# Kernel tuning notes

Measured on AMD Instinct MI355X. Metric: run time of the kernel, lower is better.

Reference implementation:

```python
import jax, jax.numpy as jnp
import numpy as np

HEADS = 16
DIM_HEAD = 64
DIM = 1024
DIM_HIDDEN = HEADS * DIM_HEAD


def setup_inputs() -> dict:
    key = jax.random.key(0)
    ks = jax.random.split(key, 5)
    b, n = 4, 2048
    x = jax.random.normal(ks[0], (b, n, DIM), dtype=jnp.float32)
    # nn.Linear weights stored as [out, in]; init ~ U(-1/sqrt(in), 1/sqrt(in))
    s = 1.0 / np.sqrt(DIM)
    w_q = jax.random.uniform(ks[1], (DIM_HIDDEN, DIM), minval=-s, maxval=s, dtype=jnp.float32)
    w_kv = jax.random.uniform(ks[2], (2 * DIM_HIDDEN, DIM), minval=-s, maxval=s, dtype=jnp.float32)
    so = 1.0 / np.sqrt(DIM_HIDDEN)
    w_out = jax.random.uniform(ks[3], (DIM, DIM_HIDDEN), minval=-so, maxval=so, dtype=jnp.float32)
    b_out = jax.random.uniform(ks[4], (DIM,), minval=-so, maxval=so, dtype=jnp.float32)
    return {"x": x, "w_q": w_q, "w_kv": w_kv, "w_out": w_out, "b_out": b_out}


def reference(x, w_q, w_kv, w_out, b_out):
    b, n, _ = x.shape
    h, e = HEADS, DIM_HEAD
    q = x @ w_q.T                     # [b, n, h*e]
    kv = x @ w_kv.T                   # [b, n, 2*h*e]
    k, v = jnp.split(kv, 2, axis=-1)
    split = lambda t: t.reshape(b, n, h, e).transpose(0, 2, 1, 3)  # [b, h, n, e]
    q, k, v = split(q), split(k), split(v)
    scale = e ** (-0.5)
    energy = jnp.einsum('bhie,bhje->bhij', q, k) * scale
    attn_w = jax.nn.softmax(energy, axis=-1)
    attn = jnp.einsum('bhij,bhje->bhie', attn_w, v)  # [b, h, n, e]
    out = attn.transpose(0, 2, 1, 3).reshape(b, n, h * e)
    return out @ w_out.T + b_out
```

## Files before the change

kernel.cpp:

```cpp
#include <hip/hip_runtime.h>

typedef __attribute__((ext_vector_type(8))) short bf16x8;
typedef __attribute__((ext_vector_type(4))) float f32x4;

#define AS1 __attribute__((address_space(1)))
#define AS3 __attribute__((address_space(3)))

#if defined(__has_builtin)
#  if __has_builtin(__builtin_amdgcn_exp2f)
#    define EXP2F(x) __builtin_amdgcn_exp2f(x)
#  endif
#endif
#ifndef EXP2F
#  define EXP2F(x) __builtin_exp2f(x)
#endif

#define BAR_WAIT_VM8  asm volatile("s_waitcnt vmcnt(8)\ns_barrier" ::: "memory")
#define BAR_WAIT_VM4  asm volatile("s_waitcnt vmcnt(4)\ns_barrier" ::: "memory")
#define BAR_WAIT_VM2  asm volatile("s_waitcnt vmcnt(2)\ns_barrier" ::: "memory")
#define BAR_WAIT_VM0  asm volatile("s_waitcnt vmcnt(0)\ns_barrier" ::: "memory")
#define BAR_WAIT_LGKM asm volatile("s_waitcnt lgkmcnt(0)\ns_barrier" ::: "memory")

#define PL32(a, b) asm("v_permlane32_swap_b32 %0, %1" : "+v"(a), "+v"(b))
#define PL16(a, b) asm("v_permlane16_swap_b32 %0, %1" : "+v"(a), "+v"(b))

__device__ __forceinline__ unsigned short f2bf(float f) {
    union { float f; unsigned u; } v; v.f = f;
    unsigned r = v.u + 0x7fffu + ((v.u >> 16) & 1u);
    return (unsigned short)(r >> 16);
}

__device__ __forceinline__ void dma16(const void* g, void* l) {
    __builtin_amdgcn_global_load_lds((const AS1 unsigned int*)g,
                                     (AS3 unsigned int*)l, 16, 0, 0);
}

__global__ __launch_bounds__(256) void convert_regions(
    const float* __restrict__ s0, unsigned short* __restrict__ d0, int n0, float c0,
    const float* __restrict__ s1, unsigned short* __restrict__ d1, int n1, float c1,
    const float* __restrict__ s2, unsigned short* __restrict__ d2, int n2, float c2)
{
    long long e = ((long long)blockIdx.x * 256 + threadIdx.x) * 8;
    const float* s; unsigned short* d; float sc;
    if (e < n0) { s = s0; d = d0; sc = c0; }
    else { e -= n0;
    if (e < n1) { s = s1; d = d1; sc = c1; }
    else { e -= n1;
    if (e < n2) { s = s2; d = d2; sc = c2; } else return; } }
    const float4 f0 = *(const float4*)(s + e);
    const float4 f1 = *(const float4*)(s + e + 4);
    union { unsigned short u[8]; uint4 q; } t;
    t.u[0]=f2bf(f0.x*sc); t.u[1]=f2bf(f0.y*sc); t.u[2]=f2bf(f0.z*sc); t.u[3]=f2bf(f0.w*sc);
    t.u[4]=f2bf(f1.x*sc); t.u[5]=f2bf(f1.y*sc); t.u[6]=f2bf(f1.z*sc); t.u[7]=f2bf(f1.w*sc);
    *(uint4*)(d + e) = t.q;
}

template<int CM>
__global__ __launch_bounds__(256) void gemm128(
    const unsigned short* __restrict__ A, const unsigned short* __restrict__ B,
    void* __restrict__ C0, void* __restrict__ C1, void* __restrict__ C2,
    const float* __restrict__ bias, int M, int N, int K)
{
    __shared__ __align__(16) unsigned short smem[2 * 16384];

    const int tid  = threadIdx.x;
    const int wq   = tid >> 6;
    const int lane = tid & 63;
    const int l16  = lane & 15;
    const int quad = lane >> 4;
    const int m0   = blockIdx.x * 128;
    const int n0   = blockIdx.y * 128;
    const int lr   = lane >> 3;
    const int cs   = lane & 7;
    const bool vswap = (CM == 1) && (n0 >= 2048);

    f32x4 acc[4][4];
#pragma unroll
    for (int mt = 0; mt < 4; ++mt)
#pragma unroll
        for (int nt = 0; nt < 4; ++nt) acc[mt][nt] = (f32x4){0.f, 0.f, 0.f, 0.f};

    auto issue = [&](int buf, int kk) {
        unsigned short* as = smem + buf * 16384;
        unsigned short* bs = as + 8192;
#pragma unroll
        for (int i = 0; i < 4; ++i) {
            const int rr = (wq * 4 + i) * 8 + lr;
            const int cg = cs ^ (rr & 7);
            dma16(A + (size_t)(m0 + rr) * K + kk + cg * 8, as + (wq * 4 + i) * 512);
            dma16(B + (size_t)(n0 + rr) * K + kk + cg * 8, bs + (wq * 4 + i) * 512);
        }
    };

    const int nIt = K >> 6;
    issue(0, 0);
#pragma unroll 2
    for (int it = 0; it < nIt; ++it) {
        const int cur = it & 1;
        if (it + 1 < nIt) {
            issue(cur ^ 1, (it + 1) << 6);
            BAR_WAIT_VM8;
        } else {
            BAR_WAIT_VM0;
        }
        const unsigned short* as = smem + cur * 16384;
        const unsigned short* bs = as + 8192;
#pragma unroll
        for (int ch = 0; ch < 2; ++ch) {
            const int swz = (((ch * 4 + quad) ^ (l16 & 7)) * 8);
            bf16x8 aF[4], bF[4];
#pragma unroll
            for (int mt = 0; mt < 4; ++mt)
                aF[mt] = *(const bf16x8*)(as + ((wq >> 1) * 64 + mt * 16 + l16) * 64 + swz);
#pragma unroll
            for (int nt = 0; nt < 4; ++nt)
                bF[nt] = *(const bf16x8*)(bs + ((wq & 1) * 64 + nt * 16 + l16) * 64 + swz);
            if (vswap) {
#pragma unroll
                for (int mt = 0; mt < 4; ++mt)
#pragma unroll
                    for (int nt = 0; nt < 4; ++nt)
                        acc[mt][nt] = __builtin_amdgcn_mfma_f32_16x16x32_bf16(
                            bF[nt], aF[mt], acc[mt][nt], 0, 0, 0);
            } else {
#pragma unroll
                for (int mt = 0; mt < 4; ++mt)
#pragma unroll
                    for (int nt = 0; nt < 4; ++nt)
                        acc[mt][nt] = __builtin_amdgcn_mfma_f32_16x16x32_bf16(
                            aF[mt], bF[nt], acc[mt][nt], 0, 0, 0);
            }
        }
        BAR_WAIT_LGKM;
    }

    const int wr = wq >> 1, wc = wq & 1;
    if (CM == 0) {
#pragma unroll
        for (int mt = 0; mt < 4; ++mt)
#pragma unroll
        for (int nt = 0; nt < 4; ++nt) {
            const int coln = n0 + wc * 64 + nt * 16 + l16;
            const float bv = bias ? bias[coln] : 0.f;
#pragma unroll
            for (int r = 0; r < 4; ++r) {
                const int rowm = m0 + wr * 64 + mt * 16 + quad * 4 + r;
                ((float*)C0)[(size_t)rowm * N + coln] = acc[mt][nt][r] + bv;
            }
        }
    } else if (!vswap) {
#pragma unroll
        for (int mt = 0; mt < 4; ++mt)
#pragma unroll
        for (int nt = 0; nt < 4; ++nt) {
            const int coln = n0 + wc * 64 + nt * 16 + l16;
            unsigned short* dst = (coln < 1024) ? (unsigned short*)C0 : (unsigned short*)C1;
            const int h = (coln >> 6) & 15, e = coln & 63;
#pragma unroll
            for (int r = 0; r < 4; ++r) {
                const int rowm = m0 + wr * 64 + mt * 16 + quad * 4 + r;
                const int b = rowm >> 11, n = rowm & 2047;
                dst[(((size_t)(b * 16 + h) * 2048 + n) << 6) + e] = f2bf(acc[mt][nt][r]);
            }
        }
    } else {
#pragma unroll
        for (int mt = 0; mt < 4; ++mt)
#pragma unroll
        for (int nt = 0; nt < 4; ++nt) {
#pragma unroll
            for (int r = 0; r < 4; ++r) {
                const int eg = n0 + wc * 64 + nt * 16 + quad * 4 + r;
                const int h = (eg >> 6) - 32, e = eg & 63;
                const int rowm = m0 + wr * 64 + mt * 16 + l16;
                const int b = rowm >> 11, n = rowm & 2047;
                ((unsigned short*)C2)[((size_t)(b * 16 + h) * 64 + e) * 2048 + n] =
                    f2bf(acc[mt][nt][r]);
            }
        }
    }
}

__global__ __launch_bounds__(512, 4) void attn_kernel(
    const unsigned short* __restrict__ Q, const unsigned short* __restrict__ K,
    const unsigned short* __restrict__ V, unsigned short* __restrict__ O)
{
    __shared__ __align__(16) unsigned short KVs[2 * 8192];

    const int tid  = threadIdx.x;
    const int q0   = blockIdx.x * 256;
    const int bh   = blockIdx.y;
    const int wq   = tid >> 6;
    const int lane = tid & 63;
    const int l16  = lane & 15;
    const int quad = lane >> 4;
    const int lr   = lane >> 3;
    const int cs   = lane & 7;
    const int swl  = l16 & 7;

    const unsigned short* Qg = Q + (size_t)bh * 2048 * 64;
    const unsigned short* Kg = K + (size_t)bh * 2048 * 64;
    const unsigned short* Vg = V + (size_t)bh * 64 * 2048;

    bf16x8 bQ[2][2];
#pragma unroll
    for (int sub = 0; sub < 2; ++sub)
#pragma unroll
        for (int ch = 0; ch < 2; ++ch)
            bQ[sub][ch] = *(const bf16x8*)(Qg + (size_t)(q0 + wq * 32 + sub * 16 + l16) * 64
                                           + ch * 32 + quad * 8);

    bf16x8 ones;
#pragma unroll
    for (int i = 0; i < 8; ++i) ones[i] = (short)0x3F80;

    f32x4 o[2][4], lf[2];
#pragma unroll
    for (int s = 0; s < 2; ++s) {
        lf[s] = (f32x4){0.f, 0.f, 0.f, 0.f};
#pragma unroll
        for (int e = 0; e < 4; ++e) o[s][e] = (f32x4){0.f, 0.f, 0.f, 0.f};
    }

    auto issueKV = [&](int buf, int key0) {
        unsigned short* ks = KVs + buf * 8192;
        unsigned short* vt = ks + 4096;
#pragma unroll
        for (int i = 0; i < 2; ++i) {
            const int j  = wq * 2 + i;
            const int rr = (j & 7) * 8 + lr;
            const int cg = cs ^ (rr & 7);
            if (j < 8)
                dma16(Kg + (size_t)(key0 + rr) * 64 + cg * 8, ks + (j & 7) * 512);
            else
                dma16(Vg + (size_t)rr * 2048 + key0 + cg * 8, vt + (j & 7) * 512);
        }
    };

    issueKV(0, 0);
#pragma unroll 2
    for (int kt = 0; kt < 32; ++kt) {
        const int cur = kt & 1;
        if (kt + 1 < 32) {
            issueKV(cur ^ 1, (kt + 1) * 64);
            BAR_WAIT_VM2;
        } else {
            BAR_WAIT_VM0;
        }
        const unsigned short* ks = KVs + cur * 8192;
        const unsigned short* vt = ks + 4096;

        f32x4 s[2][4];
#pragma unroll
        for (int sub = 0; sub < 2; ++sub)
#pragma unroll
            for (int c = 0; c < 4; ++c) s[sub][c] = (f32x4){0.f, 0.f, 0.f, 0.f};
#pragma unroll
        for (int ch = 0; ch < 2; ++ch) {
            const int swz = ((ch * 4 + quad) ^ swl) * 8;
#pragma unroll
            for (int c = 0; c < 4; ++c) {
                const bf16x8 aK = *(const bf16x8*)(ks + (c * 16 + l16) * 64 + swz);
#pragma unroll
                for (int sub = 0; sub < 2; ++sub)
                    s[sub][c] = __builtin_amdgcn_mfma_f32_16x16x32_bf16(
                        aK, bQ[sub][ch], s[sub][c], 0, 0, 0);
            }
        }

        bf16x8 aP[2][2];
#pragma unroll
        for (int sub = 0; sub < 2; ++sub) {
            unsigned pkx[4], pky[4];
#pragma unroll
            for (int c = 0; c < 4; ++c) {
                const float p0 = EXP2F(s[sub][c][0]);
                const float p1 = EXP2F(s[sub][c][1]);
                const float p2 = EXP2F(s[sub][c][2]);
                const float p3 = EXP2F(s[sub][c][3]);
                pkx[c] = __builtin_amdgcn_perm(__float_as_uint(p1), __float_as_uint(p0), 0x07060302);
                pky[c] = __builtin_amdgcn_perm(__float_as_uint(p3), __float_as_uint(p2), 0x07060302);
            }
#pragma unroll
            for (int cc = 0; cc < 2; ++cc) {
                unsigned dx = pkx[cc * 2], ex = pkx[cc * 2 + 1];
                unsigned dy = pky[cc * 2], ey = pky[cc * 2 + 1];
                PL32(dx, ex); PL32(dy, ey);
                PL16(dx, ex); PL16(dy, ey);
                union { unsigned u[4]; bf16x8 v; } t;
                t.u[0] = dx; t.u[1] = dy; t.u[2] = ex; t.u[3] = ey;
                aP[sub][cc] = t.v;
            }
        }

#pragma unroll
        for (int cc = 0; cc < 2; ++cc) {
            const int swz = ((cc * 4 + quad) ^ swl) * 8;
#pragma unroll
            for (int sub = 0; sub < 2; ++sub)
                lf[sub] = __builtin_amdgcn_mfma_f32_16x16x32_bf16(aP[sub][cc], ones, lf[sub], 0, 0, 0);
#pragma unroll
            for (int et = 0; et < 4; ++et) {
                const bf16x8 bV = *(const bf16x8*)(vt + (et * 16 + l16) * 64 + swz);
#pragma unroll
                for (int sub = 0; sub < 2; ++sub)
                    o[sub][et] = __builtin_amdgcn_mfma_f32_16x16x32_bf16(
                        aP[sub][cc], bV, o[sub][et], 0, 0, 0);
            }
        }
        BAR_WAIT_LGKM;
    }

    const int bb = bh >> 4, hh = bh & 15;
#pragma unroll
    for (int sub = 0; sub < 2; ++sub) {
#pragma unroll
        for (int r = 0; r < 4; ++r) {
            const float linv = 1.0f / lf[sub][r];
            const int qrow = q0 + wq * 32 + sub * 16 + quad * 4 + r;
#pragma unroll
            for (int et = 0; et < 4; ++et) {
                O[(size_t)(bb * 2048 + qrow) * 1024 + hh * 64 + et * 16 + l16] =
                    f2bf(o[sub][et][r] * linv);
            }
        }
    }
}

extern "C" void kernel_launch(void* const* d_in, const int* in_sizes, int n_in,
                              void* d_out, int out_size, void* d_ws, size_t ws_size,
                              hipStream_t stream) {
    const float* x     = (const float*)d_in[0];
    const float* w_q   = (const float*)d_in[1];
    const float* w_kv  = (const float*)d_in[2];
    const float* w_out = (const float*)d_in[3];
    const float* b_out = (const float*)d_in[4];
    const float CEXP = 0.125f * 1.44269504f;
    const size_t MB = 1024 * 1024;

    unsigned short* Qw    = (unsigned short*)d_ws;
    unsigned short* Kw    = (unsigned short*)((char*)d_ws + 16 * MB);
    unsigned short* Vw    = (unsigned short*)((char*)d_ws + 32 * MB);
    unsigned short* Ow    = (unsigned short*)((char*)d_ws + 48 * MB);
    unsigned short* xb    = (unsigned short*)d_out;
    unsigned short* wqkvb = (unsigned short*)((char*)d_out + 16 * MB);
    unsigned short* wob   = Qw;

    convert_regions<<<5632, 256, 0, stream>>>(
        x, xb, 8388608, 1.0f,
        w_q, wqkvb, 1048576, CEXP,
        w_kv, wqkvb + (size_t)1048576, 2097152, 1.0f);

    gemm128<1><<<dim3(64, 24), 256, 0, stream>>>(
        xb, wqkvb, Qw, Kw, Vw, nullptr, 8192, 3072, 1024);

    attn_kernel<<<dim3(8, 64), 512, 0, stream>>>(Qw, Kw, Vw, Ow);

    convert_regions<<<512, 256, 0, stream>>>(
        w_out, wob, 1048576, 1.0f,
        nullptr, nullptr, 0, 0.f, nullptr, nullptr, 0, 0.f);

    gemm128<0><<<dim3(64, 8), 256, 0, stream>>>(
        Ow, wob, d_out, nullptr, nullptr, b_out, 8192, 1024, 1024);
}
```

Before: 242.8 us.

## Halve attention query tile per block and remap grid for XCD-aware head locality

The attention kernel now handles 128 query rows per block (16 per wave) instead of 256, which doubles the grid to 1024 blocks and halves per-wave accumulator registers. Occupancy hints rise from 4 to 6 blocks. A 1D grid is decoded so that consecutive block IDs map to different heads in a pattern meant to keep blocks of the same head on the same XCD for K/V cache reuse. The cost is twice the K/V loads per query and fewer MFMAs per LDS read of K and V.

```diff
diff --git a/kernel.cpp b/kernel.cpp
--- a/kernel.cpp
+++ b/kernel.cpp
@@ -181,15 +181,18 @@
     }
 }
 
-__global__ __launch_bounds__(512, 4) void attn_kernel(
+__global__ __launch_bounds__(512, 6) void attn_kernel(
     const unsigned short* __restrict__ Q, const unsigned short* __restrict__ K,
     const unsigned short* __restrict__ V, unsigned short* __restrict__ O)
 {
     __shared__ __align__(16) unsigned short KVs[2 * 8192];
 
     const int tid  = threadIdx.x;
-    const int q0   = blockIdx.x * 256;
-    const int bh   = blockIdx.y;
+    const int id   = blockIdx.x;
+    const int r_   = id & 7;
+    const int s_   = id >> 3;
+    const int q0   = (s_ & 15) * 128;
+    const int bh   = r_ + 8 * (s_ >> 4);
     const int wq   = tid >> 6;
     const int lane = tid & 63;
     const int l16  = lane & 15;
@@ -202,25 +205,19 @@
     const unsigned short* Kg = K + (size_t)bh * 2048 * 64;
     const unsigned short* Vg = V + (size_t)bh * 64 * 2048;
 
-    bf16x8 bQ[2][2];
-#pragma unroll
-    for (int sub = 0; sub < 2; ++sub)
-#pragma unroll
-        for (int ch = 0; ch < 2; ++ch)
-            bQ[sub][ch] = *(const bf16x8*)(Qg + (size_t)(q0 + wq * 32 + sub * 16 + l16) * 64
-                                           + ch * 32 + quad * 8);
+    bf16x8 bQ[2];
+#pragma unroll
+    for (int ch = 0; ch < 2; ++ch)
+        bQ[ch] = *(const bf16x8*)(Qg + (size_t)(q0 + wq * 16 + l16) * 64 + ch * 32 + quad * 8);
 
     bf16x8 ones;
 #pragma unroll
     for (int i = 0; i < 8; ++i) ones[i] = (short)0x3F80;
 
-    f32x4 o[2][4], lf[2];
-#pragma unroll
-    for (int s = 0; s < 2; ++s) {
-        lf[s] = (f32x4){0.f, 0.f, 0.f, 0.f};
-#pragma unroll
-        for (int e = 0; e < 4; ++e) o[s][e] = (f32x4){0.f, 0.f, 0.f, 0.f};
-    }
+    f32x4 o[4], lf;
+    lf = (f32x4){0.f, 0.f, 0.f, 0.f};
+#pragma unroll
+    for (int e = 0; e < 4; ++e) o[e] = (f32x4){0.f, 0.f, 0.f, 0.f};
 
     auto issueKV = [&](int buf, int key0) {
         unsigned short* ks = KVs + buf * 8192;
@@ -250,34 +247,28 @@
         const unsigned short* ks = KVs + cur * 8192;
         const unsigned short* vt = ks + 4096;
 
-        f32x4 s[2][4];
-#pragma unroll
-        for (int sub = 0; sub < 2; ++sub)
-#pragma unroll
-            for (int c = 0; c < 4; ++c) s[sub][c] = (f32x4){0.f, 0.f, 0.f, 0.f};
+        f32x4 s4[4];
+#pragma unroll
+        for (int c = 0; c < 4; ++c) s4[c] = (f32x4){0.f, 0.f, 0.f, 0.f};
 #pragma unroll
         for (int ch = 0; ch < 2; ++ch) {
             const int swz = ((ch * 4 + quad) ^ swl) * 8;
 #pragma unroll
             for (int c = 0; c < 4; ++c) {
                 const bf16x8 aK = *(const bf16x8*)(ks + (c * 16 + l16) * 64 + swz);
-#pragma unroll
-                for (int sub = 0; sub < 2; ++sub)
-                    s[sub][c] = __builtin_amdgcn_mfma_f32_16x16x32_bf16(
-                        aK, bQ[sub][ch], s[sub][c], 0, 0, 0);
-            }
-        }
-
-        bf16x8 aP[2][2];
-#pragma unroll
-        for (int sub = 0; sub < 2; ++sub) {
+                s4[c] = __builtin_amdgcn_mfma_f32_16x16x32_bf16(aK, bQ[ch], s4[c], 0, 0, 0);
+            }
+        }
+
+        bf16x8 aP[2];
+        {
             unsigned pkx[4], pky[4];
 #pragma unroll
             for (int c = 0; c < 4; ++c) {
-                const float p0 = EXP2F(s[sub][c][0]);
-                const float p1 = EXP2F(s[sub][c][1]);
-                const float p2 = EXP2F(s[sub][c][2]);
-                const float p3 = EXP2F(s[sub][c][3]);
+                const float p0 = EXP2F(s4[c][0]);
+                const float p1 = EXP2F(s4[c][1]);
+                const float p2 = EXP2F(s4[c][2]);
+                const float p3 = EXP2F(s4[c][3]);
                 pkx[c] = __builtin_amdgcn_perm(__float_as_uint(p1), __float_as_uint(p0), 0x07060302);
                 pky[c] = __builtin_amdgcn_perm(__float_as_uint(p3), __float_as_uint(p2), 0x07060302);
             }
@@ -289,23 +280,18 @@
                 PL16(dx, ex); PL16(dy, ey);
                 union { unsigned u[4]; bf16x8 v; } t;
                 t.u[0] = dx; t.u[1] = dy; t.u[2] = ex; t.u[3] = ey;
-                aP[sub][cc] = t.v;
+                aP[cc] = t.v;
             }
         }
 
 #pragma unroll
         for (int cc = 0; cc < 2; ++cc) {
             const int swz = ((cc * 4 + quad) ^ swl) * 8;
-#pragma unroll
-            for (int sub = 0; sub < 2; ++sub)
-                lf[sub] = __builtin_amdgcn_mfma_f32_16x16x32_bf16(aP[sub][cc], ones, lf[sub], 0, 0, 0);
+            lf = __builtin_amdgcn_mfma_f32_16x16x32_bf16(aP[cc], ones, lf, 0, 0, 0);
 #pragma unroll
             for (int et = 0; et < 4; ++et) {
                 const bf16x8 bV = *(const bf16x8*)(vt + (et * 16 + l16) * 64 + swz);
-#pragma unroll
-                for (int sub = 0; sub < 2; ++sub)
-                    o[sub][et] = __builtin_amdgcn_mfma_f32_16x16x32_bf16(
-                        aP[sub][cc], bV, o[sub][et], 0, 0, 0);
+                o[et] = __builtin_amdgcn_mfma_f32_16x16x32_bf16(aP[cc], bV, o[et], 0, 0, 0);
             }
         }
         BAR_WAIT_LGKM;
@@ -313,16 +299,13 @@
 
     const int bb = bh >> 4, hh = bh & 15;
 #pragma unroll
-    for (int sub = 0; sub < 2; ++sub) {
-#pragma unroll
-        for (int r = 0; r < 4; ++r) {
-            const float linv = 1.0f / lf[sub][r];
-            const int qrow = q0 + wq * 32 + sub * 16 + quad * 4 + r;
-#pragma unroll
-            for (int et = 0; et < 4; ++et) {
-                O[(size_t)(bb * 2048 + qrow) * 1024 + hh * 64 + et * 16 + l16] =
-                    f2bf(o[sub][et][r] * linv);
-            }
+    for (int r = 0; r < 4; ++r) {
+        const float linv = 1.0f / lf[r];
+        const int qrow = q0 + wq * 16 + quad * 4 + r;
+#pragma unroll
+        for (int et = 0; et < 4; ++et) {
+            O[(size_t)(bb * 2048 + qrow) * 1024 + hh * 64 + et * 16 + l16] =
+                f2bf(o[et][r] * linv);
         }
     }
 }
@@ -354,7 +337,7 @@
     gemm128<1><<<dim3(64, 24), 256, 0, stream>>>(
         xb, wqkvb, Qw, Kw, Vw, nullptr, 8192, 3072, 1024);
 
-    attn_kernel<<<dim3(8, 64), 512, 0, stream>>>(Qw, Kw, Vw, Ow);
+    attn_kernel<<<1024, 512, 0, stream>>>(Qw, Kw, Vw, Ow);
 
     convert_regions<<<512, 256, 0, stream>>>(
         w_out, wob, 1048576, 1.0f,
```

Result: slower. 255.4 us (+5.2%).

## Permute K row mapping to drop permlane swaps and remap block grid

Applied to the files above, without the earlier changes.

The attention kernel now reads K tiles from LDS with a permuted row mapping and adjusted swizzle. The MFMA output layout then matches the P operand layout directly, so the permlane32/permlane16 swaps are removed and the packed exp values are assembled straight into bf16x8 operands. The grid is also flattened to 1D and remapped so that consecutive blocks cover different heads within groups of 8. This likely spreads work across XCDs and changes cache locality. The cost is more complex per-lane address arithmetic for the K loads, and correctness depends on the new swizzle matching the DMA write pattern.

```diff
diff --git a/kernel.cpp b/kernel.cpp
--- a/kernel.cpp
+++ b/kernel.cpp
@@ -20,9 +20,6 @@
 #define BAR_WAIT_VM2  asm volatile("s_waitcnt vmcnt(2)\ns_barrier" ::: "memory")
 #define BAR_WAIT_VM0  asm volatile("s_waitcnt vmcnt(0)\ns_barrier" ::: "memory")
 #define BAR_WAIT_LGKM asm volatile("s_waitcnt lgkmcnt(0)\ns_barrier" ::: "memory")
-
-#define PL32(a, b) asm("v_permlane32_swap_b32 %0, %1" : "+v"(a), "+v"(b))
-#define PL16(a, b) asm("v_permlane16_swap_b32 %0, %1" : "+v"(a), "+v"(b))
 
 __device__ __forceinline__ unsigned short f2bf(float f) {
     union { float f; unsigned u; } v; v.f = f;
@@ -188,8 +185,10 @@
     __shared__ __align__(16) unsigned short KVs[2 * 8192];
 
     const int tid  = threadIdx.x;
-    const int q0   = blockIdx.x * 256;
-    const int bh   = blockIdx.y;
+    const int id   = blockIdx.x;
+    const int s_   = id >> 3;
+    const int q0   = (s_ & 7) * 256;
+    const int bh   = (id & 7) + 8 * (s_ >> 3);
     const int wq   = tid >> 6;
     const int lane = tid & 63;
     const int l16  = lane & 15;
@@ -197,6 +196,9 @@
     const int lr   = lane >> 3;
     const int cs   = lane & 7;
     const int swl  = l16 & 7;
+    const int t4   = l16 & 3;
+    const int hb   = (l16 >> 2) & 1;
+    const int rA   = (l16 >> 2) * 8 + t4;
 
     const unsigned short* Qg = Q + (size_t)bh * 2048 * 64;
     const unsigned short* Kg = K + (size_t)bh * 2048 * 64;
@@ -229,11 +231,13 @@
         for (int i = 0; i < 2; ++i) {
             const int j  = wq * 2 + i;
             const int rr = (j & 7) * 8 + lr;
-            const int cg = cs ^ (rr & 7);
-            if (j < 8)
-                dma16(Kg + (size_t)(key0 + rr) * 64 + cg * 8, ks + (j & 7) * 512);
-            else
+            if (j < 8) {
+                const int cgK = cs ^ ((rr & 7) ^ (((rr >> 3) & 1) << 2));
+                dma16(Kg + (size_t)(key0 + rr) * 64 + cgK * 8, ks + (j & 7) * 512);
+            } else {
+                const int cg = cs ^ (rr & 7);
                 dma16(Vg + (size_t)rr * 2048 + key0 + cg * 8, vt + (j & 7) * 512);
+            }
         }
     };
 
@@ -257,10 +261,11 @@
             for (int c = 0; c < 4; ++c) s[sub][c] = (f32x4){0.f, 0.f, 0.f, 0.f};
 #pragma unroll
         for (int ch = 0; ch < 2; ++ch) {
-            const int swz = ((ch * 4 + quad) ^ swl) * 8;
 #pragma unroll
             for (int c = 0; c < 4; ++c) {
-                const bf16x8 aK = *(const bf16x8*)(ks + (c * 16 + l16) * 64 + swz);
+                const int row = (c >> 1) * 32 + (c & 1) * 4 + rA;
+                const int un  = (ch * 4 + quad) ^ (t4 + 4 * ((c & 1) ^ hb));
+                const bf16x8 aK = *(const bf16x8*)(ks + row * 64 + un * 8);
 #pragma unroll
                 for (int sub = 0; sub < 2; ++sub)
                     s[sub][c] = __builtin_amdgcn_mfma_f32_16x16x32_bf16(
@@ -281,16 +286,11 @@
                 pkx[c] = __builtin_amdgcn_perm(__float_as_uint(p1), __float_as_uint(p0), 0x07060302);
                 pky[c] = __builtin_amdgcn_perm(__float_as_uint(p3), __float_as_uint(p2), 0x07060302);
             }
-#pragma unroll
-            for (int cc = 0; cc < 2; ++cc) {
-                unsigned dx = pkx[cc * 2], ex = pkx[cc * 2 + 1];
-                unsigned dy = pky[cc * 2], ey = pky[cc * 2 + 1];
-                PL32(dx, ex); PL32(dy, ey);
-                PL16(dx, ex); PL16(dy, ey);
-                union { unsigned u[4]; bf16x8 v; } t;
-                t.u[0] = dx; t.u[1] = dy; t.u[2] = ex; t.u[3] = ey;
-                aP[sub][cc] = t.v;
-            }
+            union { unsigned u[4]; bf16x8 v; } lo, hi;
+            lo.u[0] = pkx[0]; lo.u[1] = pky[0]; lo.u[2] = pkx[1]; lo.u[3] = pky[1];
+            hi.u[0] = pkx[2]; hi.u[1] = pky[2]; hi.u[2] = pkx[3]; hi.u[3] = pky[3];
+            aP[sub][0] = lo.v;
+            aP[sub][1] = hi.v;
         }
 
 #pragma unroll
@@ -354,7 +354,7 @@
     gemm128<1><<<dim3(64, 24), 256, 0, stream>>>(
         xb, wqkvb, Qw, Kw, Vw, nullptr, 8192, 3072, 1024);
 
-    attn_kernel<<<dim3(8, 64), 512, 0, stream>>>(Qw, Kw, Vw, Ow);
+    attn_kernel<<<512, 512, 0, stream>>>(Qw, Kw, Vw, Ow);
 
     convert_regions<<<512, 256, 0, stream>>>(
         w_out, wob, 1048576, 1.0f,
```

Measured after the change: 246.8 us. No clear change (+1.6%).
